# Kernel optimization log

Measured on AMD Instinct MI355X. Metric: run time of the kernel, lower is better.

Reference implementation:

```python
import jax, jax.numpy as jnp
import numpy as np

N_NODES = 100000
N_EDGES = 1600000
NODE_F = 128
EDGE_F = 64
OUT = 32
NEG_SLOPE = 0.01  # torch nn.LeakyReLU default


def setup_inputs() -> dict:
    key = jax.random.key(0)
    ks = jax.random.split(key, 7)
    h = jax.random.normal(ks[0], (N_NODES, NODE_F), dtype=jnp.float32)
    edge_feat = jax.random.normal(ks[1], (N_EDGES, EDGE_F), dtype=jnp.float32)
    src = jax.random.randint(ks[2], (N_EDGES,), 0, N_NODES)
    dst = jax.random.randint(ks[3], (N_EDGES,), 0, N_NODES)
    W_node = jax.random.normal(ks[4], (NODE_F, OUT), dtype=jnp.float32) * 0.05
    W_edge = jax.random.normal(ks[5], (EDGE_F, OUT), dtype=jnp.float32) * 0.05
    attn_w = jax.random.normal(ks[6], (3 * OUT,), dtype=jnp.float32) * 0.05
    return {"h": h, "edge_feat": edge_feat, "src": src, "dst": dst,
            "W_node": W_node, "W_edge": W_edge, "attn_w": attn_w}


def reference(h, edge_feat, src, dst, W_node, W_edge, attn_w):
    # Project node and edge features (bias-free linears).
    z = h @ W_node                      # [N, OUT]
    ez = edge_feat @ W_edge             # [E, OUT]

    # attn_fc on cat(src_z, dst_z, edge_z): split weight vector to avoid
    # materializing the [E, 3*OUT] concat.
    a_src, a_dst, a_edge = attn_w[:OUT], attn_w[OUT:2 * OUT], attn_w[2 * OUT:]
    zs = z[src]                         # [E, OUT] gather
    logits = jax.nn.leaky_relu(
        zs @ a_src + z[dst] @ a_dst + ez @ a_edge, NEG_SLOPE)  # [E]

    # Per-destination (segment) softmax over incoming edges.
    seg_max = jax.ops.segment_max(logits, dst, num_segments=N_NODES)
    seg_max = jnp.where(jnp.isfinite(seg_max), seg_max, 0.0)  # empty segments
    e = jnp.exp(logits - seg_max[dst])                          # [E]
    denom = jax.ops.segment_sum(e, dst, num_segments=N_NODES)  # [N]

    # Weighted sum of src z vectors per destination.
    num = jax.ops.segment_sum(e[:, None] * zs, dst, num_segments=N_NODES)
    u = num / jnp.maximum(denom, 1e-20)[:, None]                # [N, OUT]
    return u
```

## Files before the change

kernel.cpp:

```cpp
#include <hip/hip_runtime.h>
#include <hip/hip_bf16.h>

#define N_NODES 100000
#define N_EDGES 1600000
#define NODE_F 128
#define EDGE_F 64
#define OUT_F 32
#define NEG_SLOPE 0.01f

__device__ __forceinline__ unsigned short f2bf(float f) {
    unsigned u = __float_as_uint(f);
    unsigned r = u + 0x7fffu + ((u >> 16) & 1u);
    return (unsigned short)(r >> 16);
}
__device__ __forceinline__ float bf2f(unsigned short b) {
    return __uint_as_float((unsigned)b << 16);
}

__global__ void k_node_proj(const float* __restrict__ h,
                            const float* __restrict__ W_node,
                            const float* __restrict__ attn_w,
                            unsigned short* __restrict__ zb,
                            float* __restrict__ s_src,
                            float* __restrict__ s_dst) {
    __shared__ float Ws[NODE_F * OUT_F];
    for (int i = threadIdx.x; i < NODE_F * OUT_F; i += 256)
        Ws[i] = W_node[i];
    __syncthreads();

    int node = blockIdx.x * 8 + (threadIdx.x >> 5);
    int o = threadIdx.x & 31;
    if (node >= N_NODES) return;

    const float* hrow = h + (size_t)node * NODE_F;
    float acc = 0.f;
#pragma unroll 8
    for (int j = 0; j < NODE_F; ++j)
        acc += hrow[j] * Ws[j * OUT_F + o];

    zb[(size_t)node * OUT_F + o] = f2bf(acc);

    float ps = acc * attn_w[o];
    float pd = acc * attn_w[OUT_F + o];
#pragma unroll
    for (int m = 16; m >= 1; m >>= 1) {
        ps += __shfl_xor(ps, m);
        pd += __shfl_xor(pd, m);
    }
    if (o == 0) {
        s_src[node] = ps;
        s_dst[node] = pd;
    }
}

__global__ void k_edge_dot(const float* __restrict__ edge_feat,
                           const int* __restrict__ dst,
                           const float* __restrict__ W_edge,
                           const float* __restrict__ attn_w,
                           float* __restrict__ g,
                           int* __restrict__ deg) {
    __shared__ float we_s[EDGE_F];
    if (threadIdx.x < EDGE_F) {
        float a = 0.f;
#pragma unroll
        for (int kk = 0; kk < OUT_F; ++kk)
            a += W_edge[threadIdx.x * OUT_F + kk] * attn_w[2 * OUT_F + kk];
        we_s[threadIdx.x] = a;
    }
    __syncthreads();

    int t = blockIdx.x * 256 + threadIdx.x;
    int e = t >> 2;
    int sub = t & 3;
    if (e >= N_EDGES) return;

    const float4* row = (const float4*)(edge_feat + (size_t)e * EDGE_F);
    float acc = 0.f;
#pragma unroll
    for (int i = 0; i < 4; ++i) {
        int fi = sub + i * 4;
        float4 v = row[fi];
        int b = fi * 4;
        acc += v.x * we_s[b] + v.y * we_s[b + 1] + v.z * we_s[b + 2] + v.w * we_s[b + 3];
    }
    acc += __shfl_xor(acc, 1);
    acc += __shfl_xor(acc, 2);

    if (sub == 0) {
        g[e] = acc;
        atomicAdd(deg + dst[e], 1);
    }
}

__global__ void k_scan_block(const int* __restrict__ deg,
                             int* __restrict__ offs,
                             int* __restrict__ bsum) {
    __shared__ int wsum[4];
    int i = blockIdx.x * 256 + threadIdx.x;
    int lane = threadIdx.x & 63;
    int wid = threadIdx.x >> 6;
    int v = (i < N_NODES) ? deg[i] : 0;
    int x = v;
#pragma unroll
    for (int d = 1; d < 64; d <<= 1) {
        int y = __shfl_up(x, d);
        if (lane >= d) x += y;
    }
    if (lane == 63) wsum[wid] = x;
    __syncthreads();
    int add = 0;
    for (int w = 0; w < wid; ++w) add += wsum[w];
    int incl = x + add;
    if (i < N_NODES) offs[i] = incl - v;
    if (threadIdx.x == 255) bsum[blockIdx.x] = incl;
}

__global__ void k_scan_bsums(int* __restrict__ bsum, int nb) {
    __shared__ int wsum[8];
    int t = threadIdx.x;
    int lane = t & 63;
    int wid = t >> 6;
    int v = (t < nb) ? bsum[t] : 0;
    int x = v;
#pragma unroll
    for (int d = 1; d < 64; d <<= 1) {
        int y = __shfl_up(x, d);
        if (lane >= d) x += y;
    }
    if (lane == 63) wsum[wid] = x;
    __syncthreads();
    int add = 0;
    for (int w = 0; w < wid; ++w) add += wsum[w];
    int incl = x + add;
    if (t < nb) bsum[t] = incl - v;
}

__global__ void k_scan_add(int* __restrict__ offs,
                           const int* __restrict__ bsum,
                           int* __restrict__ cursor) {
    int i = blockIdx.x * 256 + threadIdx.x;
    if (i < N_NODES) {
        int o = offs[i] + bsum[blockIdx.x];
        offs[i] = o;
        cursor[i] = o;
    }
}

__global__ void k_scatter(const int* __restrict__ src,
                          const int* __restrict__ dst,
                          const float* __restrict__ g,
                          const float* __restrict__ s_src,
                          const float* __restrict__ s_dst,
                          int* __restrict__ cursor,
                          int4* __restrict__ perm4) {
    int e = blockIdx.x * 256 + threadIdx.x;
    if (e >= N_EDGES) return;
    int s = src[e], d = dst[e];
    float logit = s_src[s] + s_dst[d] + g[e];
    logit = logit > 0.f ? logit : NEG_SLOPE * logit;
    float ev = __expf(logit);
    int pos = atomicAdd(cursor + d, 1);
    perm4[pos] = make_int4(s, __float_as_int(ev), d, 0);
}

__global__ __launch_bounds__(256) void k_aggr_pos(
    const int4* __restrict__ perm4,
    const unsigned short* __restrict__ zb,
    const int* __restrict__ offs,
    const int* __restrict__ endp,
    float* __restrict__ gnum,
    float* __restrict__ gden,
    float* __restrict__ out) {
    int grp = blockIdx.x * 8 + (threadIdx.x >> 5);
    int k = threadIdx.x & 31;
    int ebase = grp * 32;

    float acc = 0.f, den = 0.f;
    int cur = perm4[ebase].z;

#pragma unroll
    for (int j = 0; j < 32; ++j) {
        int4 pj = perm4[ebase + j];
        if (pj.z != cur) {
            int st = offs[cur];
            if (st >= ebase) {
                out[(size_t)cur * OUT_F + k] = acc / fmaxf(den, 1e-20f);
            } else {
                atomicAdd(&gnum[(size_t)cur * OUT_F + k], acc);
                if (k == 0) atomicAdd(&gden[cur], den);
            }
            acc = 0.f;
            den = 0.f;
            cur = pj.z;
        }
        float evj = __int_as_float(pj.y);
        acc += evj * bf2f(zb[(size_t)pj.x * OUT_F + k]);
        den += evj;
    }
    {
        int st = offs[cur], en = endp[cur];
        if (st >= ebase && en <= ebase + 32) {
            out[(size_t)cur * OUT_F + k] = acc / fmaxf(den, 1e-20f);
        } else {
            atomicAdd(&gnum[(size_t)cur * OUT_F + k], acc);
            if (k == 0) atomicAdd(&gden[cur], den);
        }
    }
}

__global__ void k_finalize(const int* __restrict__ offs,
                           const int* __restrict__ endp,
                           const float* __restrict__ gnum,
                           const float* __restrict__ gden,
                           float* __restrict__ out) {
    int node = blockIdx.x * 8 + (threadIdx.x >> 5);
    int k = threadIdx.x & 31;
    if (node >= N_NODES) return;
    int st = offs[node], en = endp[node];
    if (st == en) {
        out[(size_t)node * OUT_F + k] = 0.f;
        return;
    }
    if ((st >> 5) != ((en - 1) >> 5))
        out[(size_t)node * OUT_F + k] =
            gnum[(size_t)node * OUT_F + k] / fmaxf(gden[node], 1e-20f);
}

extern "C" void kernel_launch(void* const* d_in, const int* in_sizes, int n_in,
                              void* d_out, int out_size, void* d_ws, size_t ws_size,
                              hipStream_t stream) {
    const float* h         = (const float*)d_in[0];
    const float* edge_feat = (const float*)d_in[1];
    const int*   src       = (const int*)d_in[2];
    const int*   dst       = (const int*)d_in[3];
    const float* W_node    = (const float*)d_in[4];
    const float* W_edge    = (const float*)d_in[5];
    const float* attn_w    = (const float*)d_in[6];
    float* out = (float*)d_out;

    char* ws = (char*)d_ws;
    size_t off = 0;
    auto alloc = [&](size_t bytes) {
        void* p = ws + off;
        off += (bytes + 255) & ~(size_t)255;
        return p;
    };
    unsigned short* zb = (unsigned short*)alloc((size_t)N_NODES * OUT_F * sizeof(unsigned short));
    float* s_src  = (float*)alloc((size_t)N_NODES * sizeof(float));
    float* s_dst  = (float*)alloc((size_t)N_NODES * sizeof(float));
    float* g      = (float*)alloc((size_t)N_EDGES * sizeof(float));
    int*   offs   = (int*)alloc((size_t)N_NODES * sizeof(int));
    int*   cursor = (int*)alloc((size_t)N_NODES * sizeof(int));
    int*   bsum   = (int*)alloc(1024 * sizeof(int));
    int4*  perm4  = (int4*)alloc((size_t)N_EDGES * sizeof(int4));
    char*  zero_base = ws + off;
    int*   deg    = (int*)alloc((size_t)N_NODES * sizeof(int));
    float* gden   = (float*)alloc((size_t)N_NODES * sizeof(float));
    float* gnum   = (float*)alloc((size_t)N_NODES * OUT_F * sizeof(float));
    size_t zero_bytes = (ws + off) - zero_base;

    const int NB = (N_NODES + 255) / 256;

    hipMemsetAsync(zero_base, 0, zero_bytes, stream);

    k_node_proj<<<(N_NODES + 7) / 8, 256, 0, stream>>>(h, W_node, attn_w, zb, s_src, s_dst);

    {
        int total = N_EDGES * 4;
        k_edge_dot<<<(total + 255) / 256, 256, 0, stream>>>(edge_feat, dst, W_edge, attn_w, g, deg);
    }
    k_scan_block<<<NB, 256, 0, stream>>>(deg, offs, bsum);
    k_scan_bsums<<<1, 512, 0, stream>>>(bsum, NB);
    k_scan_add<<<NB, 256, 0, stream>>>(offs, bsum, cursor);

    k_scatter<<<(N_EDGES + 255) / 256, 256, 0, stream>>>(
        src, dst, g, s_src, s_dst, cursor, perm4);

    k_aggr_pos<<<N_EDGES / 32 / 8, 256, 0, stream>>>(
        perm4, zb, offs, cursor, gnum, gden, out);

    k_finalize<<<(N_NODES + 7) / 8, 256, 0, stream>>>(
        offs, cursor, gnum, gden, out);
}
```

Baseline: 329.6 us.

## Fuse edge dot into scatter, shrink perm records, find chunk nodes by binary search

Splits out a degree histogram so the edge-feature dot product can be fused with the logit/exp/scatter step, which removes the intermediate g array and one pass over it. Permutation records shrink from int4 to int2 by dropping the stored destination. The aggregation kernel now learns each chunk's starting node from a new binary-search kernel and walks node boundaries through endp instead. The memset is replaced by a custom zero kernel. In exchange there is an extra pass over dst and extra small kernels, and the loop in aggregation now depends on endp reads.

```diff
diff --git a/kernel.cpp b/kernel.cpp
--- a/kernel.cpp
+++ b/kernel.cpp
@@ -7,6 +7,7 @@
 #define EDGE_F 64
 #define OUT_F 32
 #define NEG_SLOPE 0.01f
+#define N_CHUNKS (N_EDGES / 32)
 
 __device__ __forceinline__ unsigned short f2bf(float f) {
     unsigned u = __float_as_uint(f);
@@ -15,6 +16,12 @@
 }
 __device__ __forceinline__ float bf2f(unsigned short b) {
     return __uint_as_float((unsigned)b << 16);
+}
+
+__global__ void k_zero(uint4* __restrict__ p, int n16) {
+    int i = blockIdx.x * 256 + threadIdx.x;
+    int stride = gridDim.x * 256;
+    for (; i < n16; i += stride) p[i] = make_uint4(0, 0, 0, 0);
 }
 
 __global__ void k_node_proj(const float* __restrict__ h,
@@ -53,43 +60,9 @@
     }
 }
 
-__global__ void k_edge_dot(const float* __restrict__ edge_feat,
-                           const int* __restrict__ dst,
-                           const float* __restrict__ W_edge,
-                           const float* __restrict__ attn_w,
-                           float* __restrict__ g,
-                           int* __restrict__ deg) {
-    __shared__ float we_s[EDGE_F];
-    if (threadIdx.x < EDGE_F) {
-        float a = 0.f;
-#pragma unroll
-        for (int kk = 0; kk < OUT_F; ++kk)
-            a += W_edge[threadIdx.x * OUT_F + kk] * attn_w[2 * OUT_F + kk];
-        we_s[threadIdx.x] = a;
-    }
-    __syncthreads();
-
-    int t = blockIdx.x * 256 + threadIdx.x;
-    int e = t >> 2;
-    int sub = t & 3;
-    if (e >= N_EDGES) return;
-
-    const float4* row = (const float4*)(edge_feat + (size_t)e * EDGE_F);
-    float acc = 0.f;
-#pragma unroll
-    for (int i = 0; i < 4; ++i) {
-        int fi = sub + i * 4;
-        float4 v = row[fi];
-        int b = fi * 4;
-        acc += v.x * we_s[b] + v.y * we_s[b + 1] + v.z * we_s[b + 2] + v.w * we_s[b + 3];
-    }
-    acc += __shfl_xor(acc, 1);
-    acc += __shfl_xor(acc, 2);
-
-    if (sub == 0) {
-        g[e] = acc;
-        atomicAdd(deg + dst[e], 1);
-    }
+__global__ void k_hist(const int* __restrict__ dst, int* __restrict__ deg) {
+    int e = blockIdx.x * 256 + threadIdx.x;
+    if (e < N_EDGES) atomicAdd(deg + dst[e], 1);
 }
 
 __global__ void k_scan_block(const int* __restrict__ deg,
@@ -146,28 +119,70 @@
     }
 }
 
-__global__ void k_scatter(const int* __restrict__ src,
-                          const int* __restrict__ dst,
-                          const float* __restrict__ g,
-                          const float* __restrict__ s_src,
-                          const float* __restrict__ s_dst,
-                          int* __restrict__ cursor,
-                          int4* __restrict__ perm4) {
-    int e = blockIdx.x * 256 + threadIdx.x;
+__global__ void k_chunk_node(const int* __restrict__ offs, int* __restrict__ cnode) {
+    int c = blockIdx.x * 256 + threadIdx.x;
+    if (c >= N_CHUNKS) return;
+    int pos = c * 32;
+    int lo = 0, hi = N_NODES;
+    while (hi - lo > 1) {
+        int mid = (lo + hi) >> 1;
+        if (offs[mid] <= pos) lo = mid; else hi = mid;
+    }
+    cnode[c] = lo;
+}
+
+__global__ void k_edge_fused(const float* __restrict__ edge_feat,
+                             const int* __restrict__ src,
+                             const int* __restrict__ dst,
+                             const float* __restrict__ W_edge,
+                             const float* __restrict__ attn_w,
+                             const float* __restrict__ s_src,
+                             const float* __restrict__ s_dst,
+                             int* __restrict__ cursor,
+                             int2* __restrict__ perm2) {
+    __shared__ float we_s[EDGE_F];
+    if (threadIdx.x < EDGE_F) {
+        float a = 0.f;
+#pragma unroll
+        for (int kk = 0; kk < OUT_F; ++kk)
+            a += W_edge[threadIdx.x * OUT_F + kk] * attn_w[2 * OUT_F + kk];
+        we_s[threadIdx.x] = a;
+    }
+    __syncthreads();
+
+    int t = blockIdx.x * 256 + threadIdx.x;
+    int e = t >> 2;
+    int sub = t & 3;
     if (e >= N_EDGES) return;
-    int s = src[e], d = dst[e];
-    float logit = s_src[s] + s_dst[d] + g[e];
-    logit = logit > 0.f ? logit : NEG_SLOPE * logit;
-    float ev = __expf(logit);
-    int pos = atomicAdd(cursor + d, 1);
-    perm4[pos] = make_int4(s, __float_as_int(ev), d, 0);
+
+    const float4* row = (const float4*)(edge_feat + (size_t)e * EDGE_F);
+    float acc = 0.f;
+#pragma unroll
+    for (int i = 0; i < 4; ++i) {
+        int fi = sub + i * 4;
+        float4 v = row[fi];
+        int b = fi * 4;
+        acc += v.x * we_s[b] + v.y * we_s[b + 1] + v.z * we_s[b + 2] + v.w * we_s[b + 3];
+    }
+    acc += __shfl_xor(acc, 1);
+    acc += __shfl_xor(acc, 2);
+
+    if (sub == 0) {
+        int s = src[e], d = dst[e];
+        float logit = s_src[s] + s_dst[d] + acc;
+        logit = logit > 0.f ? logit : NEG_SLOPE * logit;
+        float ev = __expf(logit);
+        int p = atomicAdd(cursor + d, 1);
+        perm2[p] = make_int2(s, __float_as_int(ev));
+    }
 }
 
 __global__ __launch_bounds__(256) void k_aggr_pos(
-    const int4* __restrict__ perm4,
+    const int2* __restrict__ perm2,
     const unsigned short* __restrict__ zb,
     const int* __restrict__ offs,
     const int* __restrict__ endp,
+    const int* __restrict__ cnode,
     float* __restrict__ gnum,
     float* __restrict__ gden,
     float* __restrict__ out) {
@@ -175,15 +190,16 @@
     int k = threadIdx.x & 31;
     int ebase = grp * 32;
 
+    int cur = cnode[grp];
+    int end_cur = endp[cur];
+    bool started_in = (offs[cur] >= ebase);
     float acc = 0.f, den = 0.f;
-    int cur = perm4[ebase].z;
-
-#pragma unroll
+    int pos = ebase;
+
+#pragma unroll 8
     for (int j = 0; j < 32; ++j) {
-        int4 pj = perm4[ebase + j];
-        if (pj.z != cur) {
-            int st = offs[cur];
-            if (st >= ebase) {
+        if (pos == end_cur) {
+            if (started_in) {
                 out[(size_t)cur * OUT_F + k] = acc / fmaxf(den, 1e-20f);
             } else {
                 atomicAdd(&gnum[(size_t)cur * OUT_F + k], acc);
@@ -191,20 +207,21 @@
             }
             acc = 0.f;
             den = 0.f;
-            cur = pj.z;
+            do { ++cur; } while (endp[cur] == pos);
+            end_cur = endp[cur];
+            started_in = true;
         }
+        int2 pj = perm2[pos];
         float evj = __int_as_float(pj.y);
         acc += evj * bf2f(zb[(size_t)pj.x * OUT_F + k]);
         den += evj;
-    }
-    {
-        int st = offs[cur], en = endp[cur];
-        if (st >= ebase && en <= ebase + 32) {
-            out[(size_t)cur * OUT_F + k] = acc / fmaxf(den, 1e-20f);
-        } else {
-            atomicAdd(&gnum[(size_t)cur * OUT_F + k], acc);
-            if (k == 0) atomicAdd(&gden[cur], den);
-        }
+        ++pos;
+    }
+    if (started_in && end_cur <= ebase + 32) {
+        out[(size_t)cur * OUT_F + k] = acc / fmaxf(den, 1e-20f);
+    } else {
+        atomicAdd(&gnum[(size_t)cur * OUT_F + k], acc);
+        if (k == 0) atomicAdd(&gden[cur], den);
     }
 }
 
@@ -248,36 +265,37 @@
     unsigned short* zb = (unsigned short*)alloc((size_t)N_NODES * OUT_F * sizeof(unsigned short));
     float* s_src  = (float*)alloc((size_t)N_NODES * sizeof(float));
     float* s_dst  = (float*)alloc((size_t)N_NODES * sizeof(float));
-    float* g      = (float*)alloc((size_t)N_EDGES * sizeof(float));
     int*   offs   = (int*)alloc((size_t)N_NODES * sizeof(int));
     int*   cursor = (int*)alloc((size_t)N_NODES * sizeof(int));
     int*   bsum   = (int*)alloc(1024 * sizeof(int));
-    int4*  perm4  = (int4*)alloc((size_t)N_EDGES * sizeof(int4));
+    int*   cnode  = (int*)alloc((size_t)N_CHUNKS * sizeof(int));
+    int2*  perm2  = (int2*)alloc((size_t)N_EDGES * sizeof(int2));
     char*  zero_base = ws + off;
     int*   deg    = (int*)alloc((size_t)N_NODES * sizeof(int));
     float* gden   = (float*)alloc((size_t)N_NODES * sizeof(float));
     float* gnum   = (float*)alloc((size_t)N_NODES * OUT_F * sizeof(float));
-    size_t zero_bytes = (ws + off) - zero_base;
+    size_t zero_bytes = (size_t)((ws + off) - zero_base);
 
     const int NB = (N_NODES + 255) / 256;
 
-    hipMemsetAsync(zero_base, 0, zero_bytes, stream);
+    k_zero<<<2048, 256, 0, stream>>>((uint4*)zero_base, (int)(zero_bytes / 16));
 
     k_node_proj<<<(N_NODES + 7) / 8, 256, 0, stream>>>(h, W_node, attn_w, zb, s_src, s_dst);
 
-    {
-        int total = N_EDGES * 4;
-        k_edge_dot<<<(total + 255) / 256, 256, 0, stream>>>(edge_feat, dst, W_edge, attn_w, g, deg);
-    }
+    k_hist<<<(N_EDGES + 255) / 256, 256, 0, stream>>>(dst, deg);
     k_scan_block<<<NB, 256, 0, stream>>>(deg, offs, bsum);
     k_scan_bsums<<<1, 512, 0, stream>>>(bsum, NB);
     k_scan_add<<<NB, 256, 0, stream>>>(offs, bsum, cursor);
-
-    k_scatter<<<(N_EDGES + 255) / 256, 256, 0, stream>>>(
-        src, dst, g, s_src, s_dst, cursor, perm4);
-
-    k_aggr_pos<<<N_EDGES / 32 / 8, 256, 0, stream>>>(
-        perm4, zb, offs, cursor, gnum, gden, out);
+    k_chunk_node<<<(N_CHUNKS + 255) / 256, 256, 0, stream>>>(offs, cnode);
+
+    {
+        int total = N_EDGES * 4;
+        k_edge_fused<<<(total + 255) / 256, 256, 0, stream>>>(
+            edge_feat, src, dst, W_edge, attn_w, s_src, s_dst, cursor, perm2);
+    }
+
+    k_aggr_pos<<<N_CHUNKS / 8, 256, 0, stream>>>(
+        perm2, zb, offs, cursor, cnode, gnum, gden, out);
 
     k_finalize<<<(N_NODES + 7) / 8, 256, 0, stream>>>(
         offs, cursor, gnum, gden, out);
```

Result: slower. 394.7 us (+19.8%).
